# Kernel optimization log

Hardware: AMD Instinct MI355X
Metric: run time of the kernel (lower is better)

The kernel has to match this reference:

```python
import jax, jax.numpy as jnp
import numpy as np

B = 16384
IN_DIM = 1280
BELLY = 1024   # int(scale_dim * belly_expand)
SCALE = 512
NBINS = 100
NPAT = 10
TAU = 0.25
BASE = 3.0
LEVELS = 12


def setup_inputs() -> dict:
    key = jax.random.key(0)
    ks = jax.random.split(key, 10)
    def w(i, shape, fan_in):
        return jax.random.normal(ks[i], shape, jnp.float32) * (0.5 / np.sqrt(fan_in))
    return {
        "features": jax.random.normal(ks[0], (B, IN_DIM), jnp.float32),
        "timesteps": jax.random.randint(ks[1], (B,), 0, 1000, jnp.int32),
        "W1": w(2, (IN_DIM, BELLY), IN_DIM),
        "b1": jnp.zeros((BELLY,), jnp.float32),
        "W2": w(3, (BELLY, SCALE), BELLY),            # no bias (bias=False)
        "Wt": w(4, (SCALE, NBINS), SCALE),
        "bt": jnp.zeros((NBINS,), jnp.float32),
        "Wp": w(5, (SCALE, NBINS * NPAT), SCALE),
        "bp": jnp.zeros((NBINS * NPAT,), jnp.float32),
        "w_pos": w(6, (SCALE, 1), SCALE),             # cantor feature_to_position
        "b_pos": jnp.zeros((1,), jnp.float32),
        "alpha": jnp.float32(0.5),
    }


def cantor_staircase(z, positions, w_pos, b_pos, alpha):
    # z: [B, SCALE] normalized features; positions: [B] int timestep bins
    centers = jnp.array([0.5, 1.5, 2.5], jnp.float32)
    max_pos = positions.max() + 1
    denom = jnp.maximum(max_pos - 1, 1).astype(jnp.float32)
    pos_f = positions.astype(jnp.float32)
    x_base = jnp.where(max_pos > 1, pos_f / denom, pos_f)
    x_base = jnp.clip(x_base, 1e-6, 1.0 - 1e-6)
    shift = jnp.tanh((z @ w_pos)[:, 0] + b_pos[0]) * 0.3
    x0 = jnp.clip(x_base + shift, 1e-6, 1.0 - 1e-6)

    def step(carry, _):
        x, Cx, w = carry
        y = x * BASE                                   # [B]
        logits = -((y[:, None] - centers) ** 2) / (TAU + 1e-8)  # [B,3]
        p = jax.nn.softmax(logits, axis=-1)
        bit = p[:, 1] * alpha + p[:, 2]
        Cx = Cx + bit * w
        x = y - jnp.floor(y)
        return (x, Cx, w * 0.5), None

    (x, Cx, w), _ = jax.lax.scan(step, (x0, jnp.zeros_like(x0), jnp.float32(0.5)), None, length=LEVELS)
    return jnp.clip(Cx, 0.0, 1.0)


def reference(features, timesteps, W1, b1, W2, Wt, bt, Wp, bp, w_pos, b_pos, alpha):
    # projection: Linear -> ReLU -> (dropout=identity at eval) -> Linear(no bias)
    h = jax.nn.relu(features @ W1 + b1)                # [B, BELLY]
    z = h @ W2                                         # [B, SCALE]
    z = z / jnp.maximum(jnp.linalg.norm(z, axis=-1, keepdims=True), 1e-12)
    timestep_logits = z @ Wt + bt                      # [B, NBINS]
    timestep_class = jnp.clip(
        (timesteps.astype(jnp.float32) / 1000.0 * NBINS).astype(jnp.int32), 0, NBINS - 1)
    cantor_values = cantor_staircase(z, timestep_class, w_pos, b_pos, alpha)
    pattern_logits = z @ Wp + bp                       # [B, NBINS*NPAT]
    return (z, timestep_logits, pattern_logits, timestep_class, cantor_values)
```

## Files before the change

kernel.cpp:

```cpp
#include <hip/hip_runtime.h>
#include <hip/hip_bf16.h>

#define B_ROWS 16384
#define IN_DIM 1280
#define BELLY  1024
#define SCALE  512
#define NBINS  100
#define NPTOT  1000

typedef __attribute__((ext_vector_type(8))) short short8_t;
typedef __attribute__((ext_vector_type(4))) float f32x4;

__device__ __forceinline__ unsigned short f2bf(float f) {
  union { float f; unsigned int u; } v; v.f = f;
  unsigned int r = v.u + 0x7FFFu + ((v.u >> 16) & 1u);
  return (unsigned short)(r >> 16);
}

__device__ __forceinline__ void gload16(const void* g, void* l) {
  __builtin_amdgcn_global_load_lds(
      (const __attribute__((address_space(1))) unsigned int*)g,
      (__attribute__((address_space(3))) unsigned int*)l, 16, 0, 0);
}

__global__ void cvt_f32_bf16(const float* __restrict__ in,
                             unsigned short* __restrict__ out, int n4) {
  int i = blockIdx.x * blockDim.x + threadIdx.x;
  int stride = gridDim.x * blockDim.x;
  for (; i < n4; i += stride) {
    float4 v = ((const float4*)in)[i];
    ushort4 o;
    o.x = f2bf(v.x); o.y = f2bf(v.y); o.z = f2bf(v.z); o.w = f2bf(v.w);
    ((ushort4*)out)[i] = o;
  }
}

__global__ void transpose_cvt(const float* __restrict__ in,
                              unsigned short* __restrict__ out,
                              int K, int N, int Npad) {
  __shared__ float tile[32][33];
  int k0 = blockIdx.x * 32;
  int n0 = blockIdx.y * 32;
  int tx = threadIdx.x, ty = threadIdx.y;
  #pragma unroll
  for (int r = 0; r < 32; r += 8) {
    int k = k0 + ty + r, n = n0 + tx;
    tile[ty + r][tx] = (k < K && n < N) ? in[(size_t)k * N + n] : 0.0f;
  }
  __syncthreads();
  #pragma unroll
  for (int r = 0; r < 32; r += 8) {
    int n = n0 + ty + r, k = k0 + tx;
    if (n < Npad && k < K) out[(size_t)n * K + k] = f2bf(tile[tx][ty + r]);
  }
}

__global__ void tclass_kernel(const int* __restrict__ ts, float* __restrict__ outc,
                              int* __restrict__ gmax, int n) {
  __shared__ int smax;
  if (threadIdx.x == 0) smax = 0;
  __syncthreads();
  int local = 0;
  for (int i = blockIdx.x * blockDim.x + threadIdx.x; i < n;
       i += gridDim.x * blockDim.x) {
    float v = (float)ts[i] / 1000.0f * 100.0f;
    int c = (int)v;
    c = min(max(c, 0), NBINS - 1);
    outc[i] = (float)c;
    local = max(local, c);
  }
  atomicMax(&smax, local);
  __syncthreads();
  if (threadIdx.x == 0) atomicMax(gmax, smax);
}

template<int K, int EPI>
__global__ __launch_bounds__(512, 1)
void gemm256(const unsigned short* __restrict__ A,
             const unsigned short* __restrict__ Bt,
             float* __restrict__ outF, unsigned short* __restrict__ outH,
             const float* __restrict__ bias,
             float* __restrict__ outF2, const float* __restrict__ bias2,
             int ldOut) {
  __shared__ __align__(16) unsigned short lds[65536];
  constexpr int NT = K / 64;
  static_assert(NT % 2 == 0, "NT must be even");
  const int tid  = threadIdx.x;
  const int wid  = tid >> 6;
  const int lane = tid & 63;
  const int r0 = blockIdx.x * 256;
  const int c0 = blockIdx.y * 256;

  const int srow = wid * 16 + (lane >> 3);
  const int scol = (((lane & 7) ^ (lane >> 3)) << 3);
  const unsigned short* gA = A  + (size_t)(r0 + srow) * K + scol;
  const unsigned short* gB = Bt + (size_t)(c0 + srow) * K + scol;
  const int sdst = wid * 1024;

  const int fr = lane & 15;
  const int Ah = wid >> 2;
  const int wc = (wid & 3) * 64;
  const int ca0 = ((((lane >> 4) << 4) +  0) ^ ((lane & 7) << 4)) >> 1;
  const int ca1 = ((((lane >> 4) << 4) + 64) ^ ((lane & 7) << 4)) >> 1;

  f32x4 acc[8][4] = {};
  short8_t af[4][2];
  short8_t bfr[2][2][2];

#define STAGE_(buf, mat, half, kt) do {                                        \
    const unsigned short* g_ = ((mat) == 0 ? gA : gB)                          \
        + (size_t)(half) * 128 * K + (size_t)(kt) * 64;                        \
    unsigned short* l_ = &lds[(buf) * 32768 + (mat) * 16384 + (half) * 8192 + sdst]; \
    gload16(g_, l_);                                                           \
    gload16(g_ + 8 * K, l_ + 512);                                             \
  } while (0)

#define LDA_(buf, mh) do {                                                     \
    const unsigned short* ab_ = &lds[(buf) * 32768 + Ah * 8192];               \
    _Pragma("unroll")                                                          \
    for (int mm = 0; mm < 4; ++mm) {                                           \
      int rwh_ = (mh) * 64 + mm * 16 + fr;                                     \
      af[mm][0] = *(const short8_t*)&ab_[rwh_ * 64 + ca0];                     \
      af[mm][1] = *(const short8_t*)&ab_[rwh_ * 64 + ca1];                     \
    } } while (0)

#define LDB_(buf, nh) do {                                                     \
    _Pragma("unroll")                                                          \
    for (int nn = 0; nn < 2; ++nn) {                                           \
      int brow_ = wc + ((nh) * 2 + nn) * 16;                                   \
      const unsigned short* bb_ = &lds[(buf) * 32768 + 16384 + (brow_ >> 7) * 8192]; \
      int rwh_ = (brow_ & 127) + fr;                                           \
      bfr[nh][nn][0] = *(const short8_t*)&bb_[rwh_ * 64 + ca0];                \
      bfr[nh][nn][1] = *(const short8_t*)&bb_[rwh_ * 64 + ca1];                \
    } } while (0)

#define MM_(mh, nh) do {                                                       \
    _Pragma("unroll")                                                          \
    for (int mm = 0; mm < 4; ++mm)                                             \
      _Pragma("unroll")                                                        \
      for (int nn = 0; nn < 2; ++nn) {                                         \
        acc[(mh)*4+mm][(nh)*2+nn] = __builtin_amdgcn_mfma_f32_16x16x32_bf16(   \
            af[mm][0], bfr[nh][nn][0], acc[(mh)*4+mm][(nh)*2+nn], 0, 0, 0);    \
        acc[(mh)*4+mm][(nh)*2+nn] = __builtin_amdgcn_mfma_f32_16x16x32_bf16(   \
            af[mm][1], bfr[nh][nn][1], acc[(mh)*4+mm][(nh)*2+nn], 0, 0, 0);    \
      } } while (0)

#define BAR_       __builtin_amdgcn_s_barrier()
#define LGKM0_     asm volatile("s_waitcnt lgkmcnt(0)")
#define VM4_       asm volatile("s_waitcnt vmcnt(4)" ::: "memory")
#define PRIO1_     __builtin_amdgcn_s_setprio(1)
#define PRIO0_     __builtin_amdgcn_s_setprio(0)

  STAGE_(0, 1, 0, 0); STAGE_(0, 1, 1, 0);
  STAGE_(0, 0, 0, 0); STAGE_(0, 0, 1, 0);
  STAGE_(1, 1, 0, 1); STAGE_(1, 1, 1, 1);
  VM4_;
  BAR_;

  for (int t = 0; t < NT; t += 2) {
    const int t2 = (t + 2) % NT;
    const int t3 = (t + 3) % NT;
    LDA_(0, 0); LDB_(0, 0); STAGE_(1, 0, 0, t + 1);
    BAR_; LGKM0_; PRIO1_; MM_(0, 0); PRIO0_; BAR_;
    LDB_(0, 1); STAGE_(1, 0, 1, t + 1);
    BAR_; LGKM0_; PRIO1_; MM_(0, 1); PRIO0_; BAR_;
    LDA_(0, 1); STAGE_(0, 1, 0, t2);
    BAR_; LGKM0_; PRIO1_; MM_(1, 0); PRIO0_; BAR_;
    STAGE_(0, 1, 1, t2); VM4_;
    BAR_; LGKM0_; PRIO1_; MM_(1, 1); PRIO0_; BAR_;
    LDA_(1, 0); LDB_(1, 0); STAGE_(0, 0, 0, t2);
    BAR_; LGKM0_; PRIO1_; MM_(0, 0); PRIO0_; BAR_;
    LDB_(1, 1); STAGE_(0, 0, 1, t2);
    BAR_; LGKM0_; PRIO1_; MM_(0, 1); PRIO0_; BAR_;
    LDA_(1, 1); STAGE_(1, 1, 0, t3);
    BAR_; LGKM0_; PRIO1_; MM_(1, 0); PRIO0_; BAR_;
    STAGE_(1, 1, 1, t3); VM4_;
    BAR_; LGKM0_; PRIO1_; MM_(1, 1); PRIO0_; BAR_;
  }

  asm volatile("s_waitcnt vmcnt(0)" ::: "memory");

  const int orow = (lane >> 4) * 4;
  const int wrr  = (wid >> 2) * 128;
  #pragma unroll
  for (int m = 0; m < 8; ++m) {
    #pragma unroll
    for (int n = 0; n < 4; ++n) {
      #pragma unroll
      for (int i = 0; i < 4; ++i) {
        int row = r0 + wrr + m * 16 + orow + i;
        int col = c0 + wc + n * 16 + fr;
        float v = acc[m][n][i];
        if (EPI == 0) {
          v += bias[col];
          v = fmaxf(v, 0.0f);
          outH[(size_t)row * ldOut + col] = f2bf(v);
        } else if (EPI == 1) {
          outF[(size_t)row * ldOut + col] = v;
        } else {
          if (col < NPTOT) {
            outF[(size_t)row * ldOut + col] = v + bias[col];
          } else if (col >= 1024) {
            int cc = col - 1024;
            if (cc < NBINS) outF2[(size_t)row * NBINS + cc] = v + bias2[cc];
          }
        }
      }
    }
  }
#undef STAGE_
#undef LDA_
#undef LDB_
#undef MM_
}

__global__ void norm_cantor_kernel(const float* __restrict__ zraw,
                                   float* __restrict__ zout,
                                   unsigned short* __restrict__ zb,
                                   const float* __restrict__ w_pos,
                                   const float* __restrict__ b_pos,
                                   const float* __restrict__ alpha_p,
                                   const float* __restrict__ tclassf,
                                   const int* __restrict__ gmax,
                                   float* __restrict__ cv_out) {
  int wid = threadIdx.x >> 6, lane = threadIdx.x & 63;
  int row = blockIdx.x * 4 + wid;
  const float4* zr = (const float4*)(zraw + (size_t)row * SCALE);
  const float4* wp = (const float4*)w_pos;
  float4 v0 = zr[lane];
  float4 v1 = zr[lane + 64];
  float4 c0 = wp[lane];
  float4 c1 = wp[lane + 64];
  float ss = v0.x * v0.x + v0.y * v0.y + v0.z * v0.z + v0.w * v0.w
           + v1.x * v1.x + v1.y * v1.y + v1.z * v1.z + v1.w * v1.w;
  float rd = v0.x * c0.x + v0.y * c0.y + v0.z * c0.z + v0.w * c0.w
           + v1.x * c1.x + v1.y * c1.y + v1.z * c1.z + v1.w * c1.w;
  #pragma unroll
  for (int off = 1; off < 64; off <<= 1) {
    ss += __shfl_xor(ss, off);
    rd += __shfl_xor(rd, off);
  }
  float scale = 1.0f / fmaxf(sqrtf(ss), 1e-12f);
  float4 o0, o1;
  o0.x = v0.x * scale; o0.y = v0.y * scale; o0.z = v0.z * scale; o0.w = v0.w * scale;
  o1.x = v1.x * scale; o1.y = v1.y * scale; o1.z = v1.z * scale; o1.w = v1.w * scale;
  ((float4*)(zout + (size_t)row * SCALE))[lane] = o0;
  ((float4*)(zout + (size_t)row * SCALE))[lane + 64] = o1;
  ushort4 b0, b1;
  b0.x = f2bf(o0.x); b0.y = f2bf(o0.y); b0.z = f2bf(o0.z); b0.w = f2bf(o0.w);
  b1.x = f2bf(o1.x); b1.y = f2bf(o1.y); b1.z = f2bf(o1.z); b1.w = f2bf(o1.w);
  ((ushort4*)(zb + (size_t)row * SCALE))[lane] = b0;
  ((ushort4*)(zb + (size_t)row * SCALE))[lane + 64] = b1;

  float s = rd * scale;
  float shift = tanhf(s + b_pos[0]) * 0.3f;
  int max_pos = *gmax + 1;
  float denom = (float)max(max_pos - 1, 1);
  float posf = tclassf[row];
  float x = (max_pos > 1) ? (posf / denom) : posf;
  x = fminf(fmaxf(x, 1e-6f), 1.0f - 1e-6f);
  x = x + shift;
  x = fminf(fmaxf(x, 1e-6f), 1.0f - 1e-6f);

  float alpha = alpha_p[0];
  const float inv = 1.0f / (0.25f + 1e-8f);
  float Cx = 0.0f, w = 0.5f;
  #pragma unroll
  for (int l = 0; l < 12; ++l) {
    float y = x * 3.0f;
    float d0 = y - 0.5f, d1 = y - 1.5f, d2 = y - 2.5f;
    float l0 = -(d0 * d0) * inv, l1 = -(d1 * d1) * inv, l2 = -(d2 * d2) * inv;
    float mx = fmaxf(l0, fmaxf(l1, l2));
    float e0 = __expf(l0 - mx), e1 = __expf(l1 - mx), e2 = __expf(l2 - mx);
    float bit = (e1 * alpha + e2) / (e0 + e1 + e2);
    Cx += bit * w;
    x = y - floorf(y);
    w *= 0.5f;
  }
  if (lane == 0) cv_out[row] = fminf(fmaxf(Cx, 0.0f), 1.0f);
}

extern "C" void kernel_launch(void* const* d_in, const int* in_sizes, int n_in,
                              void* d_out, int out_size, void* d_ws, size_t ws_size,
                              hipStream_t stream) {
  const float* features = (const float*)d_in[0];
  const int*   timesteps = (const int*)d_in[1];
  const float* W1 = (const float*)d_in[2];
  const float* b1 = (const float*)d_in[3];
  const float* W2 = (const float*)d_in[4];
  const float* Wt = (const float*)d_in[5];
  const float* bt = (const float*)d_in[6];
  const float* Wp = (const float*)d_in[7];
  const float* bp = (const float*)d_in[8];
  const float* w_pos = (const float*)d_in[9];
  const float* b_pos = (const float*)d_in[10];
  const float* alpha = (const float*)d_in[11];

  char* ws = (char*)d_ws;
  const size_t WS_H   = (size_t)B_ROWS * IN_DIM * 2;
  const size_t WS_ZB  = WS_H + (size_t)B_ROWS * BELLY * 2;
  const size_t WS_W1T = WS_ZB + (size_t)B_ROWS * SCALE * 2;
  const size_t WS_W2T = WS_W1T + (size_t)BELLY * IN_DIM * 2;
  const size_t WS_WCT = WS_W2T + (size_t)SCALE * BELLY * 2;
  const size_t WS_MAX = WS_WCT + (size_t)1280 * SCALE * 2;

  unsigned short* featB = (unsigned short*)(ws);
  float*          zraw  = (float*)(ws);
  unsigned short* hB    = (unsigned short*)(ws + WS_H);
  unsigned short* zB    = (unsigned short*)(ws + WS_ZB);
  unsigned short* W1T   = (unsigned short*)(ws + WS_W1T);
  unsigned short* W2T   = (unsigned short*)(ws + WS_W2T);
  unsigned short* WCT   = (unsigned short*)(ws + WS_WCT);
  int*            gmax  = (int*)(ws + WS_MAX);

  float* out  = (float*)d_out;
  float* o_z  = out;
  float* o_t  = o_z + (size_t)B_ROWS * SCALE;
  float* o_p  = o_t + (size_t)B_ROWS * NBINS;
  float* o_c  = o_p + (size_t)B_ROWS * NPTOT;
  float* o_cv = o_c + B_ROWS;

  hipMemsetAsync(gmax, 0, 4, stream);

  cvt_f32_bf16<<<2048, 256, 0, stream>>>(features, featB, B_ROWS * IN_DIM / 4);

  dim3 tb(32, 8);
  transpose_cvt<<<dim3(40, 32), tb, 0, stream>>>(W1, W1T, IN_DIM, BELLY, BELLY);
  transpose_cvt<<<dim3(32, 16), tb, 0, stream>>>(W2, W2T, BELLY, SCALE, SCALE);
  transpose_cvt<<<dim3(16, 32), tb, 0, stream>>>(Wp, WCT, SCALE, NPTOT, 1024);
  transpose_cvt<<<dim3(16, 8),  tb, 0, stream>>>(Wt, WCT + (size_t)1024 * SCALE,
                                                 SCALE, NBINS, 256);

  tclass_kernel<<<64, 256, 0, stream>>>(timesteps, o_c, gmax, B_ROWS);

  gemm256<IN_DIM, 0><<<dim3(B_ROWS / 256, BELLY / 256), 512, 0, stream>>>(
      featB, W1T, nullptr, hB, b1, nullptr, nullptr, BELLY);
  gemm256<BELLY, 1><<<dim3(B_ROWS / 256, SCALE / 256), 512, 0, stream>>>(
      hB, W2T, zraw, nullptr, nullptr, nullptr, nullptr, SCALE);

  norm_cantor_kernel<<<B_ROWS / 4, 256, 0, stream>>>(
      zraw, o_z, zB, w_pos, b_pos, alpha, o_c, gmax, o_cv);

  gemm256<SCALE, 2><<<dim3(B_ROWS / 256, 5), 512, 0, stream>>>(
      zB, WCT, o_p, nullptr, bp, o_t, bt, NPTOT);
}
```

Measured before the change: 358.9 us.

## Use smaller 128x128 MFMA GEMM for second-layer and head projections

Adds a 128x128-tile bf16 MFMA GEMM kernel with 256 threads and uses it for the W2 projection and the fused pattern/timestep head. It replaces the 256x256 kernel there, which launched only 128 blocks and left many CUs idle. The timestep-head weight padding shrinks from 256 to 128 columns, removing wasted output tiles. The new kernel is single-buffered with no swizzle, so it may suffer from load latency and LDS bank conflicts.

```diff
diff --git a/kernel.cpp b/kernel.cpp
--- a/kernel.cpp
+++ b/kernel.cpp
@@ -79,9 +79,7 @@
 void gemm256(const unsigned short* __restrict__ A,
              const unsigned short* __restrict__ Bt,
              float* __restrict__ outF, unsigned short* __restrict__ outH,
-             const float* __restrict__ bias,
-             float* __restrict__ outF2, const float* __restrict__ bias2,
-             int ldOut) {
+             const float* __restrict__ bias, int ldOut) {
   __shared__ __align__(16) unsigned short lds[65536];
   constexpr int NT = K / 64;
   static_assert(NT % 2 == 0, "NT must be even");
@@ -195,7 +193,87 @@
           v += bias[col];
           v = fmaxf(v, 0.0f);
           outH[(size_t)row * ldOut + col] = f2bf(v);
-        } else if (EPI == 1) {
+        } else {
+          outF[(size_t)row * ldOut + col] = v;
+        }
+      }
+    }
+  }
+#undef STAGE_
+#undef LDA_
+#undef LDB_
+#undef MM_
+}
+
+template<int K, int EPI>
+__global__ __launch_bounds__(256)
+void gemm128(const unsigned short* __restrict__ A,
+             const unsigned short* __restrict__ Bt,
+             float* __restrict__ outF, const float* __restrict__ bias,
+             float* __restrict__ outF2, const float* __restrict__ bias2,
+             int ldOut) {
+  __shared__ __align__(16) unsigned short As[128 * 32];
+  __shared__ __align__(16) unsigned short Bs[128 * 32];
+
+  const int tid  = threadIdx.x;
+  const int wid  = tid >> 6;
+  const int lane = tid & 63;
+  const int r0 = blockIdx.x * 128;
+  const int c0 = blockIdx.y * 128;
+
+  const int arow = lane >> 2;
+  const int acol = (lane & 3) * 8;
+  const unsigned short* gA0 = A  + (size_t)(r0 + 16 * (2 * wid + 0) + arow) * K + acol;
+  const unsigned short* gA1 = A  + (size_t)(r0 + 16 * (2 * wid + 1) + arow) * K + acol;
+  const unsigned short* gB0 = Bt + (size_t)(c0 + 16 * (2 * wid + 0) + arow) * K + acol;
+  const unsigned short* gB1 = Bt + (size_t)(c0 + 16 * (2 * wid + 1) + arow) * K + acol;
+  unsigned short* lA0 = &As[(2 * wid + 0) * 512];
+  unsigned short* lA1 = &As[(2 * wid + 1) * 512];
+  unsigned short* lB0 = &Bs[(2 * wid + 0) * 512];
+  unsigned short* lB1 = &Bs[(2 * wid + 1) * 512];
+
+  const int wr   = (wid >> 1) * 64;
+  const int wc   = (wid & 1) * 64;
+  const int fr   = lane & 15;
+  const int koff = (lane >> 4) * 8;
+
+  f32x4 acc[4][4] = {};
+
+  for (int k0 = 0; k0 < K; k0 += 32) {
+    gload16(gA0 + k0, lA0);
+    gload16(gA1 + k0, lA1);
+    gload16(gB0 + k0, lB0);
+    gload16(gB1 + k0, lB1);
+    __syncthreads();
+
+    short8_t af[4], bfr[4];
+    #pragma unroll
+    for (int m = 0; m < 4; ++m)
+      af[m] = *(const short8_t*)&As[(wr + m * 16 + fr) * 32 + koff];
+    #pragma unroll
+    for (int n = 0; n < 4; ++n)
+      bfr[n] = *(const short8_t*)&Bs[(wc + n * 16 + fr) * 32 + koff];
+
+    #pragma unroll
+    for (int m = 0; m < 4; ++m)
+      #pragma unroll
+      for (int n = 0; n < 4; ++n)
+        acc[m][n] = __builtin_amdgcn_mfma_f32_16x16x32_bf16(af[m], bfr[n], acc[m][n], 0, 0, 0);
+
+    __syncthreads();
+  }
+
+  const int orow = (lane >> 4) * 4;
+  #pragma unroll
+  for (int m = 0; m < 4; ++m) {
+    #pragma unroll
+    for (int n = 0; n < 4; ++n) {
+      #pragma unroll
+      for (int i = 0; i < 4; ++i) {
+        int row = r0 + wr + m * 16 + orow + i;
+        int col = c0 + wc + n * 16 + fr;
+        float v = acc[m][n][i];
+        if (EPI == 1) {
           outF[(size_t)row * ldOut + col] = v;
         } else {
           if (col < NPTOT) {
@@ -208,10 +286,6 @@
       }
     }
   }
-#undef STAGE_
-#undef LDA_
-#undef LDB_
-#undef MM_
 }
 
 __global__ void norm_cantor_kernel(const float* __restrict__ zraw,
@@ -328,19 +402,19 @@
   transpose_cvt<<<dim3(40, 32), tb, 0, stream>>>(W1, W1T, IN_DIM, BELLY, BELLY);
   transpose_cvt<<<dim3(32, 16), tb, 0, stream>>>(W2, W2T, BELLY, SCALE, SCALE);
   transpose_cvt<<<dim3(16, 32), tb, 0, stream>>>(Wp, WCT, SCALE, NPTOT, 1024);
-  transpose_cvt<<<dim3(16, 8),  tb, 0, stream>>>(Wt, WCT + (size_t)1024 * SCALE,
-                                                 SCALE, NBINS, 256);
+  transpose_cvt<<<dim3(16, 4),  tb, 0, stream>>>(Wt, WCT + (size_t)1024 * SCALE,
+                                                 SCALE, NBINS, 128);
 
   tclass_kernel<<<64, 256, 0, stream>>>(timesteps, o_c, gmax, B_ROWS);
 
   gemm256<IN_DIM, 0><<<dim3(B_ROWS / 256, BELLY / 256), 512, 0, stream>>>(
-      featB, W1T, nullptr, hB, b1, nullptr, nullptr, BELLY);
-  gemm256<BELLY, 1><<<dim3(B_ROWS / 256, SCALE / 256), 512, 0, stream>>>(
-      hB, W2T, zraw, nullptr, nullptr, nullptr, nullptr, SCALE);
+      featB, W1T, nullptr, hB, b1, BELLY);
+  gemm128<BELLY, 1><<<dim3(B_ROWS / 128, SCALE / 128), 256, 0, stream>>>(
+      hB, W2T, zraw, nullptr, nullptr, nullptr, SCALE);
 
   norm_cantor_kernel<<<B_ROWS / 4, 256, 0, stream>>>(
       zraw, o_z, zB, w_pos, b_pos, alpha, o_c, gmax, o_cv);
 
-  gemm256<SCALE, 2><<<dim3(B_ROWS / 256, 5), 512, 0, stream>>>(
-      zB, WCT, o_p, nullptr, bp, o_t, bt, NPTOT);
-}
+  gemm128<SCALE, 2><<<dim3(B_ROWS / 128, 9), 256, 0, stream>>>(
+      zB, WCT, o_p, bp, o_t, bt, NPTOT);
+}
```

New measurement: 346.6 us. 3.4% less time.
